# Performance work log

Measured on AMD Instinct MI355X. Metric: run time of the kernel, lower is better.

## Reference

```python
import jax, jax.numpy as jnp
import numpy as np

BINS = 32
MAX_DIST = 128
EMB = 1024
DQ = 64
DV = 64
H = 16
B = 8
L = 1024


def _t5_bucket_table():
    # matches: clamp(n,max=m) + (log(clamp(n,min=m)-m+1)*(bins-1-m)/log(max_distance-m+1)).long()
    n = np.arange(MAX_DIST + 1)
    m = BINS // 2
    idx = np.minimum(n, m) + (
        np.log(np.maximum(n, m) - m + 1) * (BINS - 1 - m) / np.log(MAX_DIST - m + 1)
    ).astype(np.int64)
    return jnp.asarray(idx)


def setup_inputs() -> dict:
    key = jax.random.key(0)
    ks = jax.random.split(key, 8)
    s = 0.02
    return {
        "x": jax.random.normal(ks[0], (B, L, EMB), dtype=jnp.float32),
        "qk_w": jax.random.normal(ks[1], (2 * DQ * H, EMB), dtype=jnp.float32) * s,
        "qk_b": jnp.zeros((2 * DQ * H,), dtype=jnp.float32),
        "v_w": jax.random.normal(ks[2], (DV * H, EMB), dtype=jnp.float32) * s,
        "v_b": jnp.zeros((DV * H,), dtype=jnp.float32),
        "out_w": jax.random.normal(ks[3], (EMB, DV * H), dtype=jnp.float32) * s,
        "out_b": jnp.zeros((EMB,), dtype=jnp.float32),
        "bias": jax.random.normal(ks[4], (BINS, H), dtype=jnp.float32) * s,  # causal -> bins rows
    }


def reference(x, qk_w, qk_b, v_w, v_b, out_w, out_b, bias):
    # projections
    qk = (x @ qk_w.T + qk_b).reshape(B, L, H, 2 * DQ).transpose(0, 2, 1, 3)  # [B,H,L,2DQ]
    q, k = qk[..., :DQ], qk[..., DQ:]
    v = (x @ v_w.T + v_b).reshape(B, L, H, DV).transpose(0, 2, 1, 3)  # [B,H,L,DV]

    # T5 relative-position bias (causal): gather per (i-j) distance bucket
    idx_tab = _t5_bucket_table()
    shifts = jnp.arange(L)[:, None] - jnp.arange(L)[None, :]  # [L,L], i - j
    bins_idx = idx_tab[jnp.clip(jnp.abs(shifts), 0, MAX_DIST)]  # [L,L]
    bmat = bias[bins_idx].transpose(2, 0, 1)  # [H,L,L]
    bmat = jnp.where(shifts < 0, -jnp.inf, bmat)  # causal mask (j > i)

    scale = 1.0 / np.sqrt(DQ).astype(np.float32)
    scores = jnp.einsum("bhid,bhjd->bhij", q, k) * scale + bmat  # [B,H,L,L]
    attn = jax.nn.softmax(scores, axis=-1)
    out = jnp.einsum("bhij,bhjd->bhid", attn, v)  # [B,H,L,DV]
    out = out.transpose(0, 2, 1, 3).reshape(B, L, H * DV)
    return out @ out_w.T + out_b
```

## Files before the change

### kernel.cpp

```cpp
#include <hip/hip_runtime.h>
#include <cmath>


typedef _Float16 f16x8 __attribute__((ext_vector_type(8)));
typedef _Float16 f16x4 __attribute__((ext_vector_type(4)));
typedef float    f32x4 __attribute__((ext_vector_type(4)));

#define NEG_INF (-__builtin_inff())
#define LOG2E 1.4426950408889634f

#if __has_builtin(__builtin_amdgcn_exp2f)
#define EXP2(x) __builtin_amdgcn_exp2f(x)
#else
#define EXP2(x) exp2f(x)
#endif

__device__ __forceinline__ void gl_lds16(const void* g, void* l) {
  __builtin_amdgcn_global_load_lds(
      (__attribute__((address_space(1))) void*)g,
      (__attribute__((address_space(3))) void*)l,
      16, 0, 0);
}

__device__ __forceinline__ f32x4 mfma32(f16x8 a, f16x8 b, f32x4 c) {
  return __builtin_amdgcn_mfma_f32_16x16x32_f16(a, b, c, 0, 0, 0);
}
__device__ __forceinline__ f32x4 mfma16(f16x4 a, f16x4 b, f32x4 c) {
  return __builtin_amdgcn_mfma_f32_16x16x16f16(a, b, c, 0, 0, 0);
}

typedef __attribute__((address_space(3))) _Float16* lds_f16p;

__global__ void cvt_kernel(const float* __restrict__ in,
                           _Float16* __restrict__ out, int n4) {
  int i = blockIdx.x * blockDim.x + threadIdx.x;
  if (i >= n4) return;
  float4 v = reinterpret_cast<const float4*>(in)[i];
  f16x4 o;
  o[0] = (_Float16)v.x; o[1] = (_Float16)v.y;
  o[2] = (_Float16)v.z; o[3] = (_Float16)v.w;
  reinterpret_cast<f16x4*>(out)[i] = o;
}

#define GEMM_VM4 asm volatile("s_waitcnt vmcnt(4)" ::: "memory")
#define GEMM_VM0 asm volatile("s_waitcnt vmcnt(0)" ::: "memory")
#define GEMM_BAR __builtin_amdgcn_s_barrier()
#define DSR(d, a, o) \
  asm volatile("ds_read_b128 %0, %1 offset:" o : "=v"(d) : "v"(a))

#define GEMM_STAGE(buf, kk)                         \
  do {                                              \
    gl_lds16(pA0 + (kk), &lds_a[buf][wofs]);        \
    gl_lds16(pA1 + (kk), &lds_a[buf][2048 + wofs]); \
    gl_lds16(pB0 + (kk), &lds_b[buf][wofs]);        \
    gl_lds16(pB1 + (kk), &lds_b[buf][2048 + wofs]); \
  } while (0)

#define GEMM_COMPUTE(aB, bB)                                     \
  do {                                                           \
    f16x8 af[4], bf[4];                                          \
    DSR(af[0], aB, "0");                                         \
    DSR(af[1], aB, "1024");                                      \
    DSR(af[2], aB, "2048");                                      \
    DSR(af[3], aB, "3072");                                      \
    DSR(bf[0], bB, "0");                                         \
    DSR(bf[1], bB, "1024");                                      \
    DSR(bf[2], bB, "2048");                                      \
    DSR(bf[3], bB, "3072");                                      \
    asm volatile("s_waitcnt lgkmcnt(0)" ::: "memory");           \
    __builtin_amdgcn_sched_barrier(0);                           \
    __builtin_amdgcn_s_setprio(1);                               \
    _Pragma("unroll") for (int mi = 0; mi < 4; ++mi)             \
        _Pragma("unroll") for (int ni = 0; ni < 4; ++ni)         \
            acc[mi][ni] = mfma32(af[mi], bf[ni], acc[mi][ni]);   \
    __builtin_amdgcn_s_setprio(0);                               \
  } while (0)

template <int MODE>
__global__ __launch_bounds__(256, 3) void gemm_kernel(
    const _Float16* __restrict__ A, const _Float16* __restrict__ Bm,
    int M, int N, int K,
    const float* __restrict__ bias_q, const float* __restrict__ bias_v,
    _Float16* __restrict__ qkbuf, _Float16* __restrict__ vtbuf,
    const float* __restrict__ bias_o, float* __restrict__ outf) {
  __shared__ __align__(16) _Float16 lds_a[2][128 * 32];
  __shared__ __align__(16) _Float16 lds_b[2][128 * 32];
  const int t = threadIdx.x;
  const int w = t >> 6;
  const int lane = t & 63;
  const int lq = lane & 15, lg = lane >> 4;
  const int wr = w >> 1, wc = w & 1;

  const int ngx = gridDim.x;
  const int nwg = ngx * gridDim.y;
  const int f = blockIdx.x + blockIdx.y * ngx;
  const int swz = (f & 7) * (nwg >> 3) + (f >> 3);
  const int bx = swz % ngx, by = swz / ngx;
  const int m0 = by * 128, n0 = bx * 128;

  const _Float16* pA0 = A + (size_t)(m0 + (t >> 2)) * K + (t & 3) * 8;
  const _Float16* pA1 = pA0 + (size_t)64 * K;
  const _Float16* pB0 = Bm + (size_t)(n0 + (t >> 2)) * K + (t & 3) * 8;
  const _Float16* pB1 = pB0 + (size_t)64 * K;
  const int wofs = w * 512;

  const uint32_t aB0 = (uint32_t)(uintptr_t)(lds_f16p)&lds_a[0][0] +
                       (uint32_t)((wr * 64 + lq) * 64 + lg * 16);
  const uint32_t aB1 = aB0 + 8192;
  const uint32_t bB0 = (uint32_t)(uintptr_t)(lds_f16p)&lds_b[0][0] +
                       (uint32_t)((wc * 64 + lq) * 64 + lg * 16);
  const uint32_t bB1 = bB0 + 8192;

  f32x4 acc[4][4];
#pragma unroll
  for (int mi = 0; mi < 4; ++mi)
#pragma unroll
    for (int ni = 0; ni < 4; ++ni) acc[mi][ni] = (f32x4){0.f, 0.f, 0.f, 0.f};

  GEMM_STAGE(0, 0);
  for (int kt = 0; kt < K - 64; kt += 64) {
    GEMM_STAGE(1, kt + 32);
    GEMM_VM4;
    GEMM_BAR;
    GEMM_COMPUTE(aB0, bB0);
    GEMM_BAR;
    GEMM_STAGE(0, kt + 64);
    GEMM_VM4;
    GEMM_BAR;
    GEMM_COMPUTE(aB1, bB1);
    GEMM_BAR;
  }
  GEMM_STAGE(1, K - 32);
  GEMM_VM4;
  GEMM_BAR;
  GEMM_COMPUTE(aB0, bB0);
  GEMM_BAR;
  GEMM_VM0;
  GEMM_BAR;
  GEMM_COMPUTE(aB1, bB1);

  if (MODE == 0) {
    const bool isqk = (n0 < 2048);
#pragma unroll
    for (int mi = 0; mi < 4; ++mi)
#pragma unroll
      for (int ni = 0; ni < 4; ++ni)
#pragma unroll
        for (int r = 0; r < 4; ++r) {
          const int mg = m0 + wr * 64 + mi * 16 + lg * 4 + r;
          const int ng = n0 + wc * 64 + ni * 16 + lq;
          const int bb = mg >> 10, ii = mg & 1023;
          float val = acc[mi][ni][r];
          if (isqk) {
            val += bias_q[ng];
            const int hh = ng >> 7, cc = ng & 127;
            qkbuf[((size_t)((bb * 16 + hh) * 1024 + ii)) * 128 + cc] =
                (_Float16)val;
          } else {
            const int nn = ng - 2048;
            val += bias_v[nn];
            const int hh = nn >> 6, dv = nn & 63;
            vtbuf[((size_t)((bb * 16 + hh) * 64 + dv)) * 1024 + ii] =
                (_Float16)val;
          }
        }
  } else {
#pragma unroll
    for (int mi = 0; mi < 4; ++mi)
#pragma unroll
      for (int ni = 0; ni < 4; ++ni)
#pragma unroll
        for (int r = 0; r < 4; ++r) {
          const int mg = m0 + wr * 64 + mi * 16 + lg * 4 + r;
          const int ng = n0 + wc * 64 + ni * 16 + lq;
          outf[(size_t)mg * N + ng] = acc[mi][ni][r] + bias_o[ng];
        }
  }
}

__device__ __forceinline__ void stage_kv(const _Float16* __restrict__ kb,
                                         const _Float16* __restrict__ vtb,
                                         int j0, _Float16* kl, _Float16* vl,
                                         int t) {
  const int r0 = t >> 3, c0 = t & 7;
  const int r1 = r0 + 32;
  const int kc0 = c0 ^ (r0 & 7), kc1 = c0 ^ (r1 & 7);
  gl_lds16(kb + (size_t)(j0 + r0) * 128 + kc0 * 8, kl + t * 8);
  gl_lds16(kb + (size_t)(j0 + r1) * 128 + kc1 * 8, kl + (t + 256) * 8);
  gl_lds16(vtb + (size_t)r0 * 1024 + j0 + kc0 * 8, vl + t * 8);
  gl_lds16(vtb + (size_t)r1 * 1024 + j0 + kc1 * 8, vl + (t + 256) * 8);
}

__device__ __forceinline__ void softmax16(f32x4 (&st)[4], f16x4 (&ph)[4],
                                          int qi, int j0, bool far,
                                          const float* __restrict__ tab,
                                          float t128, int lg4, float& m_run,
                                          float& l_part, f32x4 (&oacc)[4]) {
  float xs[16];
  float lmax = NEG_INF;
  if (far) {
#pragma unroll
    for (int js = 0; js < 4; ++js)
#pragma unroll
      for (int r = 0; r < 4; ++r) {
        const float xv = fmaf(st[js][r], 0.125f * LOG2E, t128);
        xs[js * 4 + r] = xv;
        lmax = fmaxf(lmax, xv);
      }
  } else {
#pragma unroll
    for (int js = 0; js < 4; ++js)
#pragma unroll
      for (int r = 0; r < 4; ++r) {
        const int jj = j0 + js * 16 + lg4 + r;
        const int dd = qi - jj;
        const int idx = dd < 0 ? 0 : (dd > 128 ? 128 : dd);
        const float xv =
            (dd < 0) ? NEG_INF : fmaf(st[js][r], 0.125f * LOG2E, tab[idx]);
        xs[js * 4 + r] = xv;
        lmax = fmaxf(lmax, xv);
      }
  }
  if (__any(lmax > m_run + 8.0f)) {
    float tmax = fmaxf(lmax, __shfl_xor(lmax, 16));
    tmax = fmaxf(tmax, __shfl_xor(tmax, 32));
    const float m_new = fmaxf(m_run, tmax);
    const float sf = EXP2(m_run - m_new);
    m_run = m_new;
    l_part *= sf;
    f32x4 sfv;
#pragma unroll
    for (int r = 0; r < 4; ++r) sfv[r] = __shfl(sf, lg4 + r);
#pragma unroll
    for (int db = 0; db < 4; ++db) oacc[db] *= sfv;
  }
  float ls = 0.f;
#pragma unroll
  for (int js = 0; js < 4; ++js)
#pragma unroll
    for (int r = 0; r < 4; ++r) {
      const float p = EXP2(xs[js * 4 + r] - m_run);
      ls += p;
      ph[js][r] = (_Float16)p;
    }
  l_part += ls;
}

__global__ __launch_bounds__(256, 4) void attn_kernel(
    const _Float16* __restrict__ qk,
    const _Float16* __restrict__ vt,
    const float* __restrict__ bias,
    _Float16* __restrict__ ao) {
  __shared__ __align__(16) _Float16 kls[2][64 * 64];
  __shared__ __align__(16) _Float16 vls[2][64 * 64];
  __shared__ float tab[132];
  const int t = threadIdx.x;
  const int bid = blockIdx.x;
  const int bh = (bid & 7) * 16 + (bid >> 6);
  const int b4 = (bid >> 3) & 7;
  const int h = bh & 15, b = bh >> 4;
  if (t < 129) {
    const int bucket =
        (t <= 16) ? t : 16 + (int)(log((double)(t - 15)) * 15.0 / log(113.0));
    tab[t] = bias[bucket * 16 + h] * LOG2E;
  }

  const int w = t >> 6, lane = t & 63;
  const int lq = lane & 15, lg = lane >> 4;
  const int lg4 = lg * 4, lg8 = lg * 8;
  const int tA = b4, tB = 15 - b4;
  const int q0A = tA * 64 + w * 16, q0B = tB * 64 + w * 16;
  const int qA = q0A + lq, qB = q0B + lq;
  const _Float16* qkb = qk + (size_t)bh * 1024 * 128;
  const _Float16* kb = qkb + 64;
  const _Float16* vtb = vt + (size_t)bh * 64 * 1024;

  const f16x8 qfA0 = *(const f16x8*)&qkb[qA * 128 + lg8];
  const f16x8 qfA1 = *(const f16x8*)&qkb[qA * 128 + 32 + lg8];
  const f16x8 qfB0 = *(const f16x8*)&qkb[qB * 128 + lg8];
  const f16x8 qfB1 = *(const f16x8*)&qkb[qB * 128 + 32 + lg8];

  f32x4 oA[4], oB[4];
#pragma unroll
  for (int db = 0; db < 4; ++db) {
    oA[db] = (f32x4){0.f, 0.f, 0.f, 0.f};
    oB[db] = (f32x4){0.f, 0.f, 0.f, 0.f};
  }
  float mA = NEG_INF, lAp = 0.f, mB = NEG_INF, lBp = 0.f;

  stage_kv(kb, vtb, 0, kls[0], vls[0], t);
  __syncthreads();
  const float t128 = tab[128];
  const int krsw = lq & 7;
  const int vsw = (lq & 7) << 1;
  int cur = 0;

  for (int jt = 0; jt <= tB; ++jt) {
    const int j0 = jt * 64;
    if (jt < tB) stage_kv(kb, vtb, j0 + 64, kls[cur ^ 1], vls[cur ^ 1], t);
    const bool aact = (jt <= tA);
    const _Float16* kbf = kls[cur];
    const _Float16* vbf = vls[cur];

    f32x4 stA[4], stB[4];
#pragma unroll
    for (int js = 0; js < 4; ++js) {
      const int rowb = (js * 16 + lq) * 64;
      const f16x8 kf0 = *(const f16x8*)&kbf[rowb + ((lg ^ krsw) << 3)];
      const f16x8 kf1 = *(const f16x8*)&kbf[rowb + (((lg + 4) ^ krsw) << 3)];
      if (aact) {
        stA[js] = mfma32(kf0, qfA0, (f32x4){0.f, 0.f, 0.f, 0.f});
        stA[js] = mfma32(kf1, qfA1, stA[js]);
      }
      stB[js] = mfma32(kf0, qfB0, (f32x4){0.f, 0.f, 0.f, 0.f});
      stB[js] = mfma32(kf1, qfB1, stB[js]);
    }

    f16x4 phA[4], phB[4];
    if (aact)
      softmax16(stA, phA, qA, j0, q0A - j0 >= 192, tab, t128, lg4, mA, lAp,
                oA);
    softmax16(stB, phB, qB, j0, q0B - j0 >= 192, tab, t128, lg4, mB, lBp, oB);

#pragma unroll
    for (int js = 0; js < 4; ++js)
#pragma unroll
      for (int db = 0; db < 4; ++db) {
        const f16x4 vf = *(const f16x4*)&vbf[(db * 16 + lq) * 64 +
                                             ((((js << 2) + lg) ^ vsw) << 2)];
        if (aact) oA[db] = mfma16(phA[js], vf, oA[db]);
        oB[db] = mfma16(phB[js], vf, oB[db]);
      }

    __syncthreads();
    cur ^= 1;
  }

  _Float16* aob = ao + ((size_t)b * 1024) * 1024 + h * 64;
  {
    float lt = lAp + __shfl_xor(lAp, 16);
    lt += __shfl_xor(lt, 32);
    f32x4 linv;
#pragma unroll
    for (int r = 0; r < 4; ++r) linv[r] = 1.0f / __shfl(lt, lg4 + r);
#pragma unroll
    for (int db = 0; db < 4; ++db)
#pragma unroll
      for (int r = 0; r < 4; ++r)
        aob[(size_t)(q0A + lg4 + r) * 1024 + db * 16 + lq] =
            (_Float16)(oA[db][r] * linv[r]);
  }
  {
    float lt = lBp + __shfl_xor(lBp, 16);
    lt += __shfl_xor(lt, 32);
    f32x4 linv;
#pragma unroll
    for (int r = 0; r < 4; ++r) linv[r] = 1.0f / __shfl(lt, lg4 + r);
#pragma unroll
    for (int db = 0; db < 4; ++db)
#pragma unroll
      for (int r = 0; r < 4; ++r)
        aob[(size_t)(q0B + lg4 + r) * 1024 + db * 16 + lq] =
            (_Float16)(oB[db][r] * linv[r]);
  }
}

extern "C" void kernel_launch(void* const* d_in, const int* in_sizes, int n_in,
                              void* d_out, int out_size, void* d_ws,
                              size_t ws_size, hipStream_t stream) {
  const float* x = (const float*)d_in[0];
  const float* qk_w = (const float*)d_in[1];
  const float* qk_b = (const float*)d_in[2];
  const float* v_w = (const float*)d_in[3];
  const float* v_b = (const float*)d_in[4];
  const float* out_w = (const float*)d_in[5];
  const float* out_b = (const float*)d_in[6];
  const float* bias = (const float*)d_in[7];
  float* out = (float*)d_out;

  _Float16* xb = (_Float16*)d_ws;
  _Float16* wb = xb + (size_t)8388608;
  _Float16* owb = wb + (size_t)3145728;
  _Float16* qkbuf = owb + (size_t)1048576;
  _Float16* vtbuf = qkbuf + (size_t)16777216;
  _Float16* ao = vtbuf + (size_t)8388608;

  cvt_kernel<<<8192, 256, 0, stream>>>(x, xb, 2097152);
  cvt_kernel<<<2048, 256, 0, stream>>>(qk_w, wb, 524288);
  cvt_kernel<<<1024, 256, 0, stream>>>(v_w, wb + 2097152, 262144);
  cvt_kernel<<<1024, 256, 0, stream>>>(out_w, owb, 262144);

  gemm_kernel<0><<<dim3(24, 64), 256, 0, stream>>>(
      xb, wb, 8192, 3072, 1024, qk_b, v_b, qkbuf, vtbuf, nullptr, nullptr);

  attn_kernel<<<1024, 256, 0, stream>>>(qkbuf, vtbuf, bias, ao);

  gemm_kernel<1><<<dim3(8, 64), 256, 0, stream>>>(
      ao, owb, 8192, 1024, 1024, nullptr, nullptr, nullptr, nullptr, out_b, out);
}
```

Measured before the change: 184.6 us.

## Swizzle GEMM LDS layout, interleave fragment reads with MFMAs, drop tile swizzle

The global-to-LDS staging now XOR-swizzles the 16-byte column chunk by row, and the ds_read addresses apply the matching XOR. This is meant to cut LDS bank conflicts on the 128-bit fragment reads. The compute macro interleaves A and B reads and waits only for the first half before starting the first MFMAs, so LDS latency overlaps with math. The workgroup-index swizzle for L2 locality is removed and replaced by plain blockIdx mapping, which may reduce cache reuse across tiles.

```diff
diff --git a/kernel.cpp b/kernel.cpp
--- a/kernel.cpp
+++ b/kernel.cpp
@@ -56,24 +56,39 @@
     gl_lds16(pB1 + (kk), &lds_b[buf][2048 + wofs]); \
   } while (0)
 
-#define GEMM_COMPUTE(aB, bB)                                     \
-  do {                                                           \
-    f16x8 af[4], bf[4];                                          \
-    DSR(af[0], aB, "0");                                         \
-    DSR(af[1], aB, "1024");                                      \
-    DSR(af[2], aB, "2048");                                      \
-    DSR(af[3], aB, "3072");                                      \
-    DSR(bf[0], bB, "0");                                         \
-    DSR(bf[1], bB, "1024");                                      \
-    DSR(bf[2], bB, "2048");                                      \
-    DSR(bf[3], bB, "3072");                                      \
-    asm volatile("s_waitcnt lgkmcnt(0)" ::: "memory");           \
-    __builtin_amdgcn_sched_barrier(0);                           \
-    __builtin_amdgcn_s_setprio(1);                               \
-    _Pragma("unroll") for (int mi = 0; mi < 4; ++mi)             \
-        _Pragma("unroll") for (int ni = 0; ni < 4; ++ni)         \
-            acc[mi][ni] = mfma32(af[mi], bf[ni], acc[mi][ni]);   \
-    __builtin_amdgcn_s_setprio(0);                               \
+#define GEMM_COMPUTE(aB, bB)                             \
+  do {                                                   \
+    f16x8 af0, af1, af2, af3, bf0, bf1, bf2, bf3;        \
+    DSR(af0, aB, "0");                                   \
+    DSR(bf0, bB, "0");                                   \
+    DSR(af1, aB, "1024");                                \
+    DSR(bf1, bB, "1024");                                \
+    DSR(af2, aB, "2048");                                \
+    DSR(bf2, bB, "2048");                                \
+    DSR(af3, aB, "3072");                                \
+    DSR(bf3, bB, "3072");                                \
+    asm volatile("s_waitcnt lgkmcnt(4)" ::: "memory");   \
+    __builtin_amdgcn_sched_barrier(0);                   \
+    __builtin_amdgcn_s_setprio(1);                       \
+    acc[0][0] = mfma32(af0, bf0, acc[0][0]);             \
+    acc[0][1] = mfma32(af0, bf1, acc[0][1]);             \
+    acc[1][0] = mfma32(af1, bf0, acc[1][0]);             \
+    acc[1][1] = mfma32(af1, bf1, acc[1][1]);             \
+    asm volatile("s_waitcnt lgkmcnt(0)" ::: "memory");   \
+    __builtin_amdgcn_sched_barrier(0);                   \
+    acc[0][2] = mfma32(af0, bf2, acc[0][2]);             \
+    acc[0][3] = mfma32(af0, bf3, acc[0][3]);             \
+    acc[1][2] = mfma32(af1, bf2, acc[1][2]);             \
+    acc[1][3] = mfma32(af1, bf3, acc[1][3]);             \
+    acc[2][0] = mfma32(af2, bf0, acc[2][0]);             \
+    acc[2][1] = mfma32(af2, bf1, acc[2][1]);             \
+    acc[2][2] = mfma32(af2, bf2, acc[2][2]);             \
+    acc[2][3] = mfma32(af2, bf3, acc[2][3]);             \
+    acc[3][0] = mfma32(af3, bf0, acc[3][0]);             \
+    acc[3][1] = mfma32(af3, bf1, acc[3][1]);             \
+    acc[3][2] = mfma32(af3, bf2, acc[3][2]);             \
+    acc[3][3] = mfma32(af3, bf3, acc[3][3]);             \
+    __builtin_amdgcn_s_setprio(0);                       \
   } while (0)
 
 template <int MODE>
@@ -90,25 +105,21 @@
   const int lane = t & 63;
   const int lq = lane & 15, lg = lane >> 4;
   const int wr = w >> 1, wc = w & 1;
-
-  const int ngx = gridDim.x;
-  const int nwg = ngx * gridDim.y;
-  const int f = blockIdx.x + blockIdx.y * ngx;
-  const int swz = (f & 7) * (nwg >> 3) + (f >> 3);
-  const int bx = swz % ngx, by = swz / ngx;
-  const int m0 = by * 128, n0 = bx * 128;
-
-  const _Float16* pA0 = A + (size_t)(m0 + (t >> 2)) * K + (t & 3) * 8;
+  const int m0 = blockIdx.y * 128, n0 = blockIdx.x * 128;
+
+  const int stc = ((t & 3) ^ ((t >> 3) & 3)) * 8;
+  const _Float16* pA0 = A + (size_t)(m0 + (t >> 2)) * K + stc;
   const _Float16* pA1 = pA0 + (size_t)64 * K;
-  const _Float16* pB0 = Bm + (size_t)(n0 + (t >> 2)) * K + (t & 3) * 8;
+  const _Float16* pB0 = Bm + (size_t)(n0 + (t >> 2)) * K + stc;
   const _Float16* pB1 = pB0 + (size_t)64 * K;
   const int wofs = w * 512;
 
+  const int xsw = (lq >> 1) & 3;
   const uint32_t aB0 = (uint32_t)(uintptr_t)(lds_f16p)&lds_a[0][0] +
-                       (uint32_t)((wr * 64 + lq) * 64 + lg * 16);
+                       (uint32_t)((wr * 64 + lq) * 64 + ((lg ^ xsw) << 4));
   const uint32_t aB1 = aB0 + 8192;
   const uint32_t bB0 = (uint32_t)(uintptr_t)(lds_f16p)&lds_b[0][0] +
-                       (uint32_t)((wc * 64 + lq) * 64 + lg * 16);
+                       (uint32_t)((wc * 64 + lq) * 64 + ((lg ^ xsw) << 4));
   const uint32_t bB1 = bB0 + 8192;
 
   f32x4 acc[4][4];
```

After: 184.2 us. Within noise of the previous version (-0.2%).
